# Kernel tuning notes

Hardware: AMD Instinct MI355X
Metric: run time of the kernel (lower is better)

The kernel has to match this reference:

```python
import jax, jax.numpy as jnp
import numpy as np

NUM_HEADS = 8
NUM_GROUPS = 32
EPS = 1e-5


def setup_inputs() -> dict:
    key = jax.random.key(0)
    ks = jax.random.split(key, 7)
    B, C, Hs, Ws = 8, 512, 32, 32
    x = jax.random.normal(ks[0], (B, C, Hs, Ws), jnp.float32)
    gn_w = 1.0 + 0.02 * jax.random.normal(ks[1], (C,), jnp.float32)
    gn_b = 0.02 * jax.random.normal(ks[2], (C,), jnp.float32)
    qkv_w = 0.02 * jax.random.normal(ks[3], (3 * C, C), jnp.float32)
    qkv_b = 0.02 * jax.random.normal(ks[4], (3 * C,), jnp.float32)
    proj_w = 0.02 * jax.random.normal(ks[5], (C, C), jnp.float32)
    proj_b = 0.02 * jax.random.normal(ks[6], (C,), jnp.float32)
    return {"x": x, "gn_w": gn_w, "gn_b": gn_b, "qkv_w": qkv_w,
            "qkv_b": qkv_b, "proj_w": proj_w, "proj_b": proj_b}


def reference(x, gn_w, gn_b, qkv_w, qkv_b, proj_w, proj_b):
    B, C = x.shape[0], x.shape[1]
    T = int(np.prod(x.shape[2:]))
    xr = x.reshape(B, C, T)

    # GroupNorm(32, C): normalize over (channels_per_group, T)
    g = xr.reshape(B, NUM_GROUPS, -1)
    mu = g.mean(axis=-1, keepdims=True)
    var = g.var(axis=-1, keepdims=True)
    h = ((g - mu) * jax.lax.rsqrt(var + EPS)).reshape(B, C, T)
    h = h * gn_w[:, None] + gn_b[:, None]

    # 1x1 conv -> per-position matmul: [B, 3C, T]
    qkv = jnp.einsum('oc,bct->bot', qkv_w, h) + qkv_b[:, None]

    # QKVAttention: reshape to per-head blocks of [q; k; v]
    ch = C // NUM_HEADS
    qkv = qkv.reshape(B * NUM_HEADS, 3 * ch, T)
    q, k, v = qkv[:, :ch], qkv[:, ch:2 * ch], qkv[:, 2 * ch:]
    scale = 1.0 / jnp.sqrt(jnp.sqrt(jnp.asarray(ch, q.dtype)))  # ch**-0.25
    w = jnp.einsum('bct,bcs->bts', q * scale, k * scale)        # [B*H, T, T]
    w = jax.nn.softmax(w.astype(jnp.float32), axis=-1).astype(q.dtype)
    a = jnp.einsum('bts,bcs->bct', w, v).reshape(B, C, T)

    # proj_out 1x1 conv + residual
    out = jnp.einsum('oc,bct->bot', proj_w, a) + proj_b[:, None]
    return (xr + out).reshape(x.shape)
```

## Files before the change

kernel.cpp:

```cpp
#include <hip/hip_runtime.h>
#include <hip/hip_bf16.h>

#define CCH 512
#define TTT 1024
#define BBB 8
#define NGRP 32
#define CPG 16
#define NHEAD 8
#define CHD 64
#define O_QKV 1536

typedef __attribute__((ext_vector_type(8))) short bf16x8;
typedef __attribute__((ext_vector_type(4))) short s16x4;
typedef __attribute__((ext_vector_type(8))) unsigned short u16x8;
typedef __attribute__((ext_vector_type(4))) float f32x4;

__device__ __forceinline__ float us2f(unsigned short u) {
  union { unsigned int i; float f; } p; p.i = ((unsigned int)u) << 16; return p.f;
}
__device__ __forceinline__ unsigned short f2us(float f) {
  __hip_bfloat16 b = __float2bfloat16(f);
  return *reinterpret_cast<unsigned short*>(&b);
}
__device__ __forceinline__ bf16x8 cat8(s16x4 a, s16x4 b) {
  bf16x8 r;
  r[0] = a[0]; r[1] = a[1]; r[2] = a[2]; r[3] = a[3];
  r[4] = b[0]; r[5] = b[1]; r[6] = b[2]; r[7] = b[3];
  return r;
}
__device__ __forceinline__ float hmax4(f32x4 v) {
  return fmaxf(fmaxf(v[0], v[1]), fmaxf(v[2], v[3]));
}
__device__ __forceinline__ unsigned int pk2(float lo, float hi) {
  return ((unsigned int)f2us(hi) << 16) | (unsigned int)f2us(lo);
}


__global__ __launch_bounds__(256) void wpack_kernel(
    const float* __restrict__ wq, const float* __restrict__ wp,
    unsigned short* __restrict__ op, int nslot)
{
  const int s = blockIdx.x * 256 + threadIdx.x;
  if (s >= nslot) return;
  const int u = s & 63, sub = s >> 6;
  const int kt = sub & 31, rt = sub >> 5;
  const int lg = u >> 4, lr = u & 15;
  const int row = rt * 16 + lr;
  const float* src = (row < O_QKV) ? &wq[(size_t)row * CCH]
                                   : &wp[(size_t)(row - O_QKV) * CCH];
  float4 v = *reinterpret_cast<const float4*>(&src[kt * 16 + lg * 4]);
  ushort4 r;
  r.x = f2us(v.x); r.y = f2us(v.y); r.z = f2us(v.z); r.w = f2us(v.w);
  reinterpret_cast<ushort4*>(op)[s] = r;
}

__global__ __launch_bounds__(256) void gn_kernel(
    const float* __restrict__ x,
    const float* __restrict__ gw,
    const float* __restrict__ gb,
    unsigned short* __restrict__ hP)
{
  __shared__ __align__(16) float xs[16][1028];
  const int bg = blockIdx.x;
  const int bb = bg >> 5, g = bg & 31;
  const size_t base = ((size_t)bb * CCH + (size_t)g * CPG) * TTT;
  const float4* xv = reinterpret_cast<const float4*>(x + base);
  const int tid = threadIdx.x;

  float s = 0.f, q = 0.f;
  for (int i = tid; i < 4096; i += 256) {
    float4 u = xv[i];
    const int c = i >> 8, t4 = (i & 255) << 2;
    *reinterpret_cast<float4*>(&xs[c][t4]) = u;
    s += (u.x + u.y) + (u.z + u.w);
    q += u.x * u.x + u.y * u.y + u.z * u.z + u.w * u.w;
  }
  #pragma unroll
  for (int off = 32; off > 0; off >>= 1) {
    s += __shfl_down(s, off);
    q += __shfl_down(q, off);
  }
  __shared__ float red[10];
  const int wid = tid >> 6, lane = tid & 63;
  if (lane == 0) { red[wid] = s; red[4 + wid] = q; }
  __syncthreads();
  if (tid == 0) {
    float S = red[0] + red[1] + red[2] + red[3];
    float Q = red[4] + red[5] + red[6] + red[7];
    float mu = S * (1.f / 16384.f);
    float var = Q * (1.f / 16384.f) - mu * mu;
    red[8] = mu;
    red[9] = rsqrtf(var + 1e-5f);
  }
  __syncthreads();
  const float mu = red[8], rstd = red[9];
  float wsc[16], wbs[16];
  #pragma unroll
  for (int cc = 0; cc < 16; cc++) {
    wsc[cc] = gw[g * CPG + cc] * rstd;
    wbs[cc] = gb[g * CPG + cc] - mu * wsc[cc];
  }
  for (int tt = tid; tt < 1024; tt += 256) {
    float v[16];
    #pragma unroll
    for (int cc = 0; cc < 16; cc++)
      v[cc] = fmaf(xs[cc][tt], wsc[cc], wbs[cc]);
    unsigned short* dst = &hP[(size_t)bb * 524288 + ((size_t)((tt >> 4) * 32 + g)) * 256 + (tt & 15) * 4];
    #pragma unroll
    for (int l2 = 0; l2 < 4; l2++) {
      ushort4 st;
      st.x = f2us(v[l2 * 4 + 0]);
      st.y = f2us(v[l2 * 4 + 1]);
      st.z = f2us(v[l2 * 4 + 2]);
      st.w = f2us(v[l2 * 4 + 3]);
      *reinterpret_cast<ushort4*>(&dst[l2 * 64]) = st;
    }
  }
}

template<int MODE>
__global__ __launch_bounds__(256) void gemm_p(
    const unsigned short* __restrict__ Ap,
    const unsigned short* __restrict__ Bp,
    const float* __restrict__ bias,
    const float* __restrict__ resid,
    unsigned short* __restrict__ oq,
    unsigned short* __restrict__ ok,
    unsigned short* __restrict__ ov,
    float* __restrict__ of,
    const int O)
{
  const int tid = threadIdx.x;
  const int bz = blockIdx.z, o0 = blockIdx.y << 7, t0 = blockIdx.x << 7;
  const int lane = tid & 63, w = tid >> 6;
  const int lg = lane >> 4, lr = lane & 15;
  const int wr = w >> 1, wc = w & 1;
  const int laneoff = (lg >> 1) * 256 + (lg & 1) * 128 + lr * 4;

  const unsigned short* Ab = Ap + (size_t)(((o0 >> 4) + wr * 4) * 32) * 256 + laneoff;
  const unsigned short* Bb = Bp + (size_t)bz * 524288
      + (size_t)(((t0 >> 4) + wc * 4) * 32) * 256 + laneoff;

  f32x4 acc[4][4];
  #pragma unroll
  for (int m = 0; m < 4; m++)
    #pragma unroll
    for (int n = 0; n < 4; n++) acc[m][n] = f32x4{0.f, 0.f, 0.f, 0.f};

#define LOADSET(af_, bf_, kb_) do {                                        \
    _Pragma("unroll") for (int m_ = 0; m_ < 4; m_++) {                     \
      const unsigned short* p_ = Ab + (m_ * 32 + (kb_)) * 256;             \
      af_[m_] = cat8(*reinterpret_cast<const s16x4*>(p_),                  \
                     *reinterpret_cast<const s16x4*>(p_ + 64));            \
    }                                                                      \
    _Pragma("unroll") for (int n_ = 0; n_ < 4; n_++) {                     \
      const unsigned short* p_ = Bb + (n_ * 32 + (kb_)) * 256;             \
      bf_[n_] = cat8(*reinterpret_cast<const s16x4*>(p_),                  \
                     *reinterpret_cast<const s16x4*>(p_ + 64));            \
    } } while (0)

#define MFMASET(af_, bf_) do {                                             \
    __builtin_amdgcn_s_setprio(1);                                         \
    _Pragma("unroll") for (int n_ = 0; n_ < 4; n_++)                       \
      _Pragma("unroll") for (int m_ = 0; m_ < 4; m_++)                     \
        acc[m_][n_] = __builtin_amdgcn_mfma_f32_16x16x32_bf16(             \
            af_[m_], bf_[n_], acc[m_][n_], 0, 0, 0);                       \
    __builtin_amdgcn_s_setprio(0); } while (0)

  bf16x8 afA[4], bfA[4], afB[4], bfB[4];
  LOADSET(afA, bfA, 0);
  #pragma unroll
  for (int kb = 0; kb < 32; kb += 4) {
    LOADSET(afB, bfB, kb + 2);
    MFMASET(afA, bfA);
    if (kb + 4 < 32) LOADSET(afA, bfA, kb + 4);
    MFMASET(afB, bfB);
  }
#undef LOADSET
#undef MFMASET

  if (MODE == 0) {
    const int a = (o0 >> 6) + wr;
    float bi[4][4];
    #pragma unroll
    for (int m = 0; m < 4; m++)
      #pragma unroll
      for (int r = 0; r < 4; r++)
        bi[m][r] = bias[a * 64 + m * 16 + lg * 4 + r];
    const int head = a / 3, part = a - head * 3;
    const size_t bho = ((size_t)bz * NHEAD + head) << 16;
    if (part < 2) {
      unsigned short* dst = (part == 0 ? oq : ok) + bho;
      #pragma unroll
      for (int n = 0; n < 4; n++) {
        const int rt = (t0 >> 4) + wc * 4 + n;
        #pragma unroll
        for (int m = 0; m < 4; m++) {
          ushort4 st;
          st.x = f2us(acc[m][n][0] + bi[m][0]);
          st.y = f2us(acc[m][n][1] + bi[m][1]);
          st.z = f2us(acc[m][n][2] + bi[m][2]);
          st.w = f2us(acc[m][n][3] + bi[m][3]);
          *reinterpret_cast<ushort4*>(&dst[(size_t)(rt * 4 + m) * 256 + lr * 16 + lg * 4]) = st;
        }
      }
    } else {
      unsigned short* dst = ov + bho;
      #pragma unroll
      for (int m = 0; m < 4; m++)
        #pragma unroll
        for (int n = 0; n < 4; n++) {
          const int kt = (t0 >> 4) + wc * 4 + n;
          unsigned short* q = &dst[(size_t)(m * 64 + kt) * 256 + lr];
          #pragma unroll
          for (int r = 0; r < 4; r++)
            q[(lg * 4 + r) * 16] = f2us(acc[m][n][r] + bi[m][r]);
        }
    }
  } else {
    #pragma unroll
    for (int m = 0; m < 4; m++)
      #pragma unroll
      for (int r = 0; r < 4; r++) {
        const int o = o0 + wr * 64 + m * 16 + lg * 4 + r;
        const float bv = bias[o];
        const size_t rowbase = ((size_t)bz * O + o) * TTT + t0 + wc * 64 + lr;
        #pragma unroll
        for (int n = 0; n < 4; n++) {
          const size_t idx = rowbase + n * 16;
          of[idx] = acc[m][n][r] + bv + resid[idx];
        }
      }
  }
}

__global__ __launch_bounds__(512, 3) void attn_p(
    const unsigned short* __restrict__ qP,
    const unsigned short* __restrict__ kP,
    const unsigned short* __restrict__ vP,
    unsigned short* __restrict__ avP)
{
  const int bid = blockIdx.x;
  const int bh = (bid & 7) * 8 + (bid >> 6);
  const int t0 = ((bid >> 3) & 7) << 7;
  const int b = bh >> 3, hh = bh & 7;
  const int tid = threadIdx.x;
  const int lane = tid & 63, w = tid >> 6;
  const int qg = w & 3, sh = w >> 2;
  const int lg = lane >> 4, lr = lane & 15;

  __shared__ __align__(16) unsigned char smem[4 * 64 * 37 * 4];
  unsigned short (*kv)[2][4096] = reinterpret_cast<unsigned short (*)[2][4096]>(smem);
  float (*mrg)[64][37] = reinterpret_cast<float (*)[64][37]>(smem);

  const unsigned short* Qb = qP + ((size_t)bh << 16);
  const unsigned short* Kb = kP + ((size_t)bh << 16);
  const unsigned short* Vb = vP + ((size_t)bh << 16);

  const int p = tid;
  const int swp8 = (p ^ ((p >> 4) & 1)) * 8;
  const int vsrc0 = ((p >> 7) * 64 + ((p >> 5) & 3)) * 256 + (p & 31) * 8;

  const int PLOFF = (lg >> 1) * 256 + lr * 16 + (lg & 1) * 8;
  const int hK = (lg & 1) ^ ((lr >> 2) & 1);
  const int hV = (lg & 1) ^ ((lr >> 3) & 1);
  int koff[2];
  #pragma unroll
  for (int sn = 0; sn < 2; sn++) {
    const int srow4 = (sh * 2 + (lr >> 3)) * 4 + (lg >> 1);
    const int row16 = ((lr >> 2) & 1) * 8 + sn * 4 + (lr & 3);
    koff[sn] = srow4 * 256 + row16 * 16 + hK * 8;
  }
  const int voffb = (sh * 2 + (lg >> 1)) * 256 + lr * 16 + hV * 8;

  const int rt0 = (t0 >> 4) + qg * 2;
  bf16x8 aq[2][2];
  #pragma unroll
  for (int qs = 0; qs < 2; qs++) {
    aq[qs][0] = *reinterpret_cast<const bf16x8*>(&Qb[(rt0 + qs) * 1024 + PLOFF]);
    aq[qs][1] = *reinterpret_cast<const bf16x8*>(&Qb[(rt0 + qs) * 1024 + 512 + PLOFF]);
  }

  f32x4 opv[2][4];
  #pragma unroll
  for (int qs = 0; qs < 2; qs++)
    #pragma unroll
    for (int cn = 0; cn < 4; cn++) opv[qs][cn] = f32x4{0.f, 0.f, 0.f, 0.f};
  float mrow[2] = {-1e30f, -1e30f}, lrow[2] = {0.f, 0.f};
  const float SC2 = 0.125f * 1.44269504f;

  u16x8 rK = *reinterpret_cast<const u16x8*>(&Kb[p * 8]);
  u16x8 rV = *reinterpret_cast<const u16x8*>(&Vb[vsrc0]);
  *reinterpret_cast<u16x8*>(&kv[0][0][swp8]) = rK;
  *reinterpret_cast<u16x8*>(&kv[0][1][swp8]) = rV;
  rK = *reinterpret_cast<const u16x8*>(&Kb[4096 + p * 8]);
  rV = *reinterpret_cast<const u16x8*>(&Vb[1024 + vsrc0]);

  for (int T = 0; T < 16; T++) {
    const int buf = T & 1;
    __syncthreads();
    if (T + 1 < 16) {
      *reinterpret_cast<u16x8*>(&kv[buf ^ 1][0][swp8]) = rK;
      *reinterpret_cast<u16x8*>(&kv[buf ^ 1][1][swp8]) = rV;
    }
    if (T + 2 < 16) {
      rK = *reinterpret_cast<const u16x8*>(&Kb[(T + 2) * 4096 + p * 8]);
      rV = *reinterpret_cast<const u16x8*>(&Vb[(T + 2) * 1024 + vsrc0]);
    }

    bf16x8 kf[2][2];
    #pragma unroll
    for (int sn = 0; sn < 2; sn++) {
      kf[sn][0] = *reinterpret_cast<const bf16x8*>(&kv[buf][0][koff[sn]]);
      kf[sn][1] = *reinterpret_cast<const bf16x8*>(&kv[buf][0][koff[sn] + 512]);
    }
    f32x4 sc[2][2];
    __builtin_amdgcn_s_setprio(1);
    #pragma unroll
    for (int qs = 0; qs < 2; qs++)
      #pragma unroll
      for (int sn = 0; sn < 2; sn++) {
        f32x4 t = __builtin_amdgcn_mfma_f32_16x16x32_bf16(kf[sn][0], aq[qs][0], f32x4{0.f, 0.f, 0.f, 0.f}, 0, 0, 0);
        sc[qs][sn] = __builtin_amdgcn_mfma_f32_16x16x32_bf16(kf[sn][1], aq[qs][1], t, 0, 0, 0);
      }
    __builtin_amdgcn_s_setprio(0);

    bf16x8 bv[4];
    #pragma unroll
    for (int cn = 0; cn < 4; cn++)
      bv[cn] = *reinterpret_cast<const bf16x8*>(&kv[buf][1][cn * 1024 + voffb]);

    float mx[2];
    #pragma unroll
    for (int qs = 0; qs < 2; qs++) {
      float m_ = fmaxf(hmax4(sc[qs][0]), hmax4(sc[qs][1])) * SC2;
      m_ = fmaxf(m_, __shfl_xor(m_, 16));
      mx[qs] = fmaxf(m_, __shfl_xor(m_, 32));
    }
    if (!__all(mx[0] <= mrow[0] + 8.f && mx[1] <= mrow[1] + 8.f)) {
      #pragma unroll
      for (int qs = 0; qs < 2; qs++) {
        const float mn = fmaxf(mrow[qs], mx[qs]);
        const float rsc = exp2f(mrow[qs] - mn);
        mrow[qs] = mn;
        lrow[qs] *= rsc;
        #pragma unroll
        for (int cn = 0; cn < 4; cn++)
          #pragma unroll
          for (int r = 0; r < 4; r++) opv[qs][cn][r] *= rsc;
      }
    }

    bf16x8 pb[2];
    #pragma unroll
    for (int qs = 0; qs < 2; qs++) {
      float e[8];
      float rs = 0.f;
      #pragma unroll
      for (int sn = 0; sn < 2; sn++)
        #pragma unroll
        for (int r = 0; r < 4; r++) {
          e[sn * 4 + r] = exp2f(fmaf(sc[qs][sn][r], SC2, -mrow[qs]));
          rs += e[sn * 4 + r];
        }
      lrow[qs] += rs;
      union U8 { unsigned int u[4]; bf16x8 v; } a;
      a.u[0] = pk2(e[0], e[1]); a.u[1] = pk2(e[2], e[3]);
      a.u[2] = pk2(e[4], e[5]); a.u[3] = pk2(e[6], e[7]);
      pb[qs] = a.v;
    }

    __builtin_amdgcn_s_setprio(1);
    #pragma unroll
    for (int qs = 0; qs < 2; qs++)
      #pragma unroll
      for (int cn = 0; cn < 4; cn++)
        opv[qs][cn] = __builtin_amdgcn_mfma_f32_16x16x32_bf16(bv[cn], pb[qs], opv[qs][cn], 0, 0, 0);
    __builtin_amdgcn_s_setprio(0);
  }

  float lt[2];
  #pragma unroll
  for (int qs = 0; qs < 2; qs++) {
    float v = lrow[qs];
    v += __shfl_xor(v, 16);
    v += __shfl_xor(v, 32);
    lt[qs] = v;
  }

  __syncthreads();
  if (sh == 1) {
    float* m = mrg[qg][lane];
    m[0] = mrow[0]; m[1] = mrow[1];
    m[2] = lt[0];   m[3] = lt[1];
    #pragma unroll
    for (int qs = 0; qs < 2; qs++)
      #pragma unroll
      for (int cn = 0; cn < 4; cn++)
        #pragma unroll
        for (int r = 0; r < 4; r++)
          m[4 + qs * 16 + cn * 4 + r] = opv[qs][cn][r];
  }
  __syncthreads();
  if (sh == 0) {
    const float* m = mrg[qg][lane];
    unsigned short* dst = avP + (size_t)b * 524288;
    #pragma unroll
    for (int qs = 0; qs < 2; qs++) {
      const float m2 = m[qs], l2 = m[2 + qs];
      const float mf = fmaxf(mrow[qs], m2);
      const float s1 = exp2f(mrow[qs] - mf);
      const float s2 = exp2f(m2 - mf);
      const float linv = 1.f / (lt[qs] * s1 + l2 * s2);
      const int rt = rt0 + qs;
      #pragma unroll
      for (int cn = 0; cn < 4; cn++) {
        const float* o2 = &m[4 + qs * 16 + cn * 4];
        ushort4 o;
        o.x = f2us((opv[qs][cn][0] * s1 + o2[0] * s2) * linv);
        o.y = f2us((opv[qs][cn][1] * s1 + o2[1] * s2) * linv);
        o.z = f2us((opv[qs][cn][2] * s1 + o2[2] * s2) * linv);
        o.w = f2us((opv[qs][cn][3] * s1 + o2[3] * s2) * linv);
        *reinterpret_cast<ushort4*>(&dst[((size_t)(rt * 32 + hh * 4 + cn) << 8) + lg * 64 + lr * 4]) = o;
      }
    }
  }
}

extern "C" void kernel_launch(void* const* d_in, const int* in_sizes, int n_in,
                              void* d_out, int out_size, void* d_ws, size_t ws_size,
                              hipStream_t stream) {
  const float* x      = (const float*)d_in[0];
  const float* gn_w   = (const float*)d_in[1];
  const float* gn_b   = (const float*)d_in[2];
  const float* qkv_w  = (const float*)d_in[3];
  const float* qkv_b  = (const float*)d_in[4];
  const float* proj_w = (const float*)d_in[5];
  const float* proj_b = (const float*)d_in[6];
  float* out = (float*)d_out;

  const size_t HT = (size_t)BBB * TTT * CCH;
  const size_t QK = (size_t)BBB * NHEAD * TTT * CHD;
  unsigned short* hP  = (unsigned short*)d_ws;
  unsigned short* vP  = hP + HT;
  unsigned short* avP = vP + QK;
  unsigned short* wq  = avP + HT;
  unsigned short* wp  = wq + (size_t)O_QKV * CCH;
  unsigned short* qPd = (unsigned short*)d_out;
  unsigned short* kPd = qPd + QK;

  const int nslot = (O_QKV + CCH) * CCH / 4;
  wpack_kernel<<<dim3(nslot / 256), 256, 0, stream>>>(qkv_w, proj_w, wq, nslot);
  gn_kernel<<<dim3(BBB * NGRP), 256, 0, stream>>>(x, gn_w, gn_b, hP);
  gemm_p<0><<<dim3(TTT / 128, O_QKV / 128, BBB), 256, 0, stream>>>(
      wq, hP, qkv_b, nullptr, qPd, kPd, vP, nullptr, O_QKV);
  attn_p<<<dim3(512), 512, 0, stream>>>(qPd, kPd, vP, avP);
  gemm_p<1><<<dim3(TTT / 128, CCH / 128, BBB), 256, 0, stream>>>(
      wp, avP, proj_b, x, nullptr, nullptr, nullptr, out, CCH);
}
```

Measured before the change: 93.64 us.

## Halve query rows per attention block and double grid to 1024 blocks

The attention kernel now gives each block 64 query rows instead of 128, with each wave owning one 16-row query tile instead of two. The grid doubles to 1024 blocks and launch bounds go from 3 to 4 blocks per CU, aiming for more parallelism and occupancy with fewer registers per thread. In exchange, every K/V tile is loaded from global memory and staged through LDS twice as often across the grid, lowering reuse per load.

```diff
diff --git a/kernel.cpp b/kernel.cpp
--- a/kernel.cpp
+++ b/kernel.cpp
@@ -234,24 +234,24 @@
   }
 }
 
-__global__ __launch_bounds__(512, 3) void attn_p(
+__global__ __launch_bounds__(512, 4) void attn_p(
     const unsigned short* __restrict__ qP,
     const unsigned short* __restrict__ kP,
     const unsigned short* __restrict__ vP,
     unsigned short* __restrict__ avP)
 {
   const int bid = blockIdx.x;
-  const int bh = (bid & 7) * 8 + (bid >> 6);
-  const int t0 = ((bid >> 3) & 7) << 7;
+  const int bh = (bid & 7) * 8 + ((bid >> 3) & 7);
+  const int t0 = (bid >> 6) << 6;
   const int b = bh >> 3, hh = bh & 7;
   const int tid = threadIdx.x;
   const int lane = tid & 63, w = tid >> 6;
   const int qg = w & 3, sh = w >> 2;
   const int lg = lane >> 4, lr = lane & 15;
 
-  __shared__ __align__(16) unsigned char smem[4 * 64 * 37 * 4];
+  __shared__ __align__(16) unsigned char smem[32768];
   unsigned short (*kv)[2][4096] = reinterpret_cast<unsigned short (*)[2][4096]>(smem);
-  float (*mrg)[64][37] = reinterpret_cast<float (*)[64][37]>(smem);
+  float (*mrg)[64][19] = reinterpret_cast<float (*)[64][19]>(smem);
 
   const unsigned short* Qb = qP + ((size_t)bh << 16);
   const unsigned short* Kb = kP + ((size_t)bh << 16);
@@ -273,20 +273,14 @@
   }
   const int voffb = (sh * 2 + (lg >> 1)) * 256 + lr * 16 + hV * 8;
 
-  const int rt0 = (t0 >> 4) + qg * 2;
-  bf16x8 aq[2][2];
-  #pragma unroll
-  for (int qs = 0; qs < 2; qs++) {
-    aq[qs][0] = *reinterpret_cast<const bf16x8*>(&Qb[(rt0 + qs) * 1024 + PLOFF]);
-    aq[qs][1] = *reinterpret_cast<const bf16x8*>(&Qb[(rt0 + qs) * 1024 + 512 + PLOFF]);
-  }
-
-  f32x4 opv[2][4];
-  #pragma unroll
-  for (int qs = 0; qs < 2; qs++)
-    #pragma unroll
-    for (int cn = 0; cn < 4; cn++) opv[qs][cn] = f32x4{0.f, 0.f, 0.f, 0.f};
-  float mrow[2] = {-1e30f, -1e30f}, lrow[2] = {0.f, 0.f};
+  const int rt = (t0 >> 4) + qg;
+  const bf16x8 aq0 = *reinterpret_cast<const bf16x8*>(&Qb[rt * 1024 + PLOFF]);
+  const bf16x8 aq1 = *reinterpret_cast<const bf16x8*>(&Qb[rt * 1024 + 512 + PLOFF]);
+
+  f32x4 opv[4];
+  #pragma unroll
+  for (int cn = 0; cn < 4; cn++) opv[cn] = f32x4{0.f, 0.f, 0.f, 0.f};
+  float mrow = -1e30f, lrow = 0.f;
   const float SC2 = 0.125f * 1.44269504f;
 
   u16x8 rK = *reinterpret_cast<const u16x8*>(&Kb[p * 8]);
@@ -314,15 +308,13 @@
       kf[sn][0] = *reinterpret_cast<const bf16x8*>(&kv[buf][0][koff[sn]]);
       kf[sn][1] = *reinterpret_cast<const bf16x8*>(&kv[buf][0][koff[sn] + 512]);
     }
-    f32x4 sc[2][2];
+    f32x4 sc[2];
     __builtin_amdgcn_s_setprio(1);
     #pragma unroll
-    for (int qs = 0; qs < 2; qs++)
-      #pragma unroll
-      for (int sn = 0; sn < 2; sn++) {
-        f32x4 t = __builtin_amdgcn_mfma_f32_16x16x32_bf16(kf[sn][0], aq[qs][0], f32x4{0.f, 0.f, 0.f, 0.f}, 0, 0, 0);
-        sc[qs][sn] = __builtin_amdgcn_mfma_f32_16x16x32_bf16(kf[sn][1], aq[qs][1], t, 0, 0, 0);
-      }
+    for (int sn = 0; sn < 2; sn++) {
+      f32x4 t = __builtin_amdgcn_mfma_f32_16x16x32_bf16(kf[sn][0], aq0, f32x4{0.f, 0.f, 0.f, 0.f}, 0, 0, 0);
+      sc[sn] = __builtin_amdgcn_mfma_f32_16x16x32_bf16(kf[sn][1], aq1, t, 0, 0, 0);
+    }
     __builtin_amdgcn_s_setprio(0);
 
     bf16x8 bv[4];
@@ -330,99 +322,76 @@
     for (int cn = 0; cn < 4; cn++)
       bv[cn] = *reinterpret_cast<const bf16x8*>(&kv[buf][1][cn * 1024 + voffb]);
 
-    float mx[2];
-    #pragma unroll
-    for (int qs = 0; qs < 2; qs++) {
-      float m_ = fmaxf(hmax4(sc[qs][0]), hmax4(sc[qs][1])) * SC2;
-      m_ = fmaxf(m_, __shfl_xor(m_, 16));
-      mx[qs] = fmaxf(m_, __shfl_xor(m_, 32));
-    }
-    if (!__all(mx[0] <= mrow[0] + 8.f && mx[1] <= mrow[1] + 8.f)) {
-      #pragma unroll
-      for (int qs = 0; qs < 2; qs++) {
-        const float mn = fmaxf(mrow[qs], mx[qs]);
-        const float rsc = exp2f(mrow[qs] - mn);
-        mrow[qs] = mn;
-        lrow[qs] *= rsc;
+    float mx = fmaxf(hmax4(sc[0]), hmax4(sc[1])) * SC2;
+    mx = fmaxf(mx, __shfl_xor(mx, 16));
+    mx = fmaxf(mx, __shfl_xor(mx, 32));
+    if (!__all(mx <= mrow + 8.f)) {
+      const float mn = fmaxf(mrow, mx);
+      const float rsc = exp2f(mrow - mn);
+      mrow = mn;
+      lrow *= rsc;
+      #pragma unroll
+      for (int cn = 0; cn < 4; cn++)
         #pragma unroll
-        for (int cn = 0; cn < 4; cn++)
-          #pragma unroll
-          for (int r = 0; r < 4; r++) opv[qs][cn][r] *= rsc;
+        for (int r = 0; r < 4; r++) opv[cn][r] *= rsc;
+    }
+
+    float e[8];
+    float rs = 0.f;
+    #pragma unroll
+    for (int sn = 0; sn < 2; sn++)
+      #pragma unroll
+      for (int r = 0; r < 4; r++) {
+        e[sn * 4 + r] = exp2f(fmaf(sc[sn][r], SC2, -mrow));
+        rs += e[sn * 4 + r];
       }
-    }
-
-    bf16x8 pb[2];
-    #pragma unroll
-    for (int qs = 0; qs < 2; qs++) {
-      float e[8];
-      float rs = 0.f;
-      #pragma unroll
-      for (int sn = 0; sn < 2; sn++)
-        #pragma unroll
-        for (int r = 0; r < 4; r++) {
-          e[sn * 4 + r] = exp2f(fmaf(sc[qs][sn][r], SC2, -mrow[qs]));
-          rs += e[sn * 4 + r];
-        }
-      lrow[qs] += rs;
-      union U8 { unsigned int u[4]; bf16x8 v; } a;
-      a.u[0] = pk2(e[0], e[1]); a.u[1] = pk2(e[2], e[3]);
-      a.u[2] = pk2(e[4], e[5]); a.u[3] = pk2(e[6], e[7]);
-      pb[qs] = a.v;
-    }
+    lrow += rs;
+
+    union U8 { unsigned int u[4]; bf16x8 v; } a;
+    a.u[0] = pk2(e[0], e[1]); a.u[1] = pk2(e[2], e[3]);
+    a.u[2] = pk2(e[4], e[5]); a.u[3] = pk2(e[6], e[7]);
+    const bf16x8 pb = a.v;
 
     __builtin_amdgcn_s_setprio(1);
     #pragma unroll
-    for (int qs = 0; qs < 2; qs++)
-      #pragma unroll
-      for (int cn = 0; cn < 4; cn++)
-        opv[qs][cn] = __builtin_amdgcn_mfma_f32_16x16x32_bf16(bv[cn], pb[qs], opv[qs][cn], 0, 0, 0);
+    for (int cn = 0; cn < 4; cn++)
+      opv[cn] = __builtin_amdgcn_mfma_f32_16x16x32_bf16(bv[cn], pb, opv[cn], 0, 0, 0);
     __builtin_amdgcn_s_setprio(0);
   }
 
-  float lt[2];
-  #pragma unroll
-  for (int qs = 0; qs < 2; qs++) {
-    float v = lrow[qs];
-    v += __shfl_xor(v, 16);
-    v += __shfl_xor(v, 32);
-    lt[qs] = v;
-  }
+  float lt = lrow;
+  lt += __shfl_xor(lt, 16);
+  lt += __shfl_xor(lt, 32);
 
   __syncthreads();
   if (sh == 1) {
     float* m = mrg[qg][lane];
-    m[0] = mrow[0]; m[1] = mrow[1];
-    m[2] = lt[0];   m[3] = lt[1];
-    #pragma unroll
-    for (int qs = 0; qs < 2; qs++)
-      #pragma unroll
-      for (int cn = 0; cn < 4; cn++)
-        #pragma unroll
-        for (int r = 0; r < 4; r++)
-          m[4 + qs * 16 + cn * 4 + r] = opv[qs][cn][r];
+    m[0] = mrow;
+    m[1] = lt;
+    #pragma unroll
+    for (int cn = 0; cn < 4; cn++)
+      #pragma unroll
+      for (int r = 0; r < 4; r++)
+        m[2 + cn * 4 + r] = opv[cn][r];
   }
   __syncthreads();
   if (sh == 0) {
     const float* m = mrg[qg][lane];
+    const float m2 = m[0], l2 = m[1];
+    const float mf = fmaxf(mrow, m2);
+    const float s1 = exp2f(mrow - mf);
+    const float s2 = exp2f(m2 - mf);
+    const float linv = 1.f / (lt * s1 + l2 * s2);
     unsigned short* dst = avP + (size_t)b * 524288;
     #pragma unroll
-    for (int qs = 0; qs < 2; qs++) {
-      const float m2 = m[qs], l2 = m[2 + qs];
-      const float mf = fmaxf(mrow[qs], m2);
-      const float s1 = exp2f(mrow[qs] - mf);
-      const float s2 = exp2f(m2 - mf);
-      const float linv = 1.f / (lt[qs] * s1 + l2 * s2);
-      const int rt = rt0 + qs;
-      #pragma unroll
-      for (int cn = 0; cn < 4; cn++) {
-        const float* o2 = &m[4 + qs * 16 + cn * 4];
-        ushort4 o;
-        o.x = f2us((opv[qs][cn][0] * s1 + o2[0] * s2) * linv);
-        o.y = f2us((opv[qs][cn][1] * s1 + o2[1] * s2) * linv);
-        o.z = f2us((opv[qs][cn][2] * s1 + o2[2] * s2) * linv);
-        o.w = f2us((opv[qs][cn][3] * s1 + o2[3] * s2) * linv);
-        *reinterpret_cast<ushort4*>(&dst[((size_t)(rt * 32 + hh * 4 + cn) << 8) + lg * 64 + lr * 4]) = o;
-      }
+    for (int cn = 0; cn < 4; cn++) {
+      const float* o2 = &m[2 + cn * 4];
+      ushort4 o;
+      o.x = f2us((opv[cn][0] * s1 + o2[0] * s2) * linv);
+      o.y = f2us((opv[cn][1] * s1 + o2[1] * s2) * linv);
+      o.z = f2us((opv[cn][2] * s1 + o2[2] * s2) * linv);
+      o.w = f2us((opv[cn][3] * s1 + o2[3] * s2) * linv);
+      *reinterpret_cast<ushort4*>(&dst[((size_t)(rt * 32 + hh * 4 + cn) << 8) + lg * 64 + lr * 4]) = o;
     }
   }
 }
@@ -454,7 +423,7 @@
   gn_kernel<<<dim3(BBB * NGRP), 256, 0, stream>>>(x, gn_w, gn_b, hP);
   gemm_p<0><<<dim3(TTT / 128, O_QKV / 128, BBB), 256, 0, stream>>>(
       wq, hP, qkv_b, nullptr, qPd, kPd, vP, nullptr, O_QKV);
-  attn_p<<<dim3(512), 512, 0, stream>>>(qPd, kPd, vP, avP);
+  attn_p<<<dim3(1024), 512, 0, stream>>>(qPd, kPd, vP, avP);
   gemm_p<1><<<dim3(TTT / 128, CCH / 128, BBB), 256, 0, stream>>>(
       wp, avP, proj_b, x, nullptr, nullptr, nullptr, out, CCH);
 }
```

Measured after the change: 96.34 us. 2.9% more time.
